# Kernel tuning notes

Hardware: AMD Instinct MI355X
Metric: run time of the kernel (lower is better)

## Reference

```python
import jax, jax.numpy as jnp
import numpy as np

EMBED_DIM = 1024
NUM_HEADS = 16
HEAD_DIM = EMBED_DIM // NUM_HEADS
SEQ = 2048
BATCH = 2


def setup_inputs() -> dict:
    key = jax.random.key(0)
    ks = jax.random.split(key, 8)
    s = 1.0 / np.sqrt(EMBED_DIM)
    return {
        "query": jax.random.normal(ks[0], (SEQ, BATCH, EMBED_DIM), jnp.float32),
        "key": jax.random.normal(ks[1], (SEQ, BATCH, EMBED_DIM), jnp.float32),
        "value": jax.random.normal(ks[2], (SEQ, BATCH, EMBED_DIM), jnp.float32),
        "Wq": jax.random.normal(ks[3], (EMBED_DIM, EMBED_DIM), jnp.float32) * s,
        "Wk": jax.random.normal(ks[4], (EMBED_DIM, EMBED_DIM), jnp.float32) * s,
        "Wv": jax.random.normal(ks[5], (EMBED_DIM, EMBED_DIM), jnp.float32) * s,
        "in_bias": jnp.zeros((3 * EMBED_DIM,), jnp.float32),
        "Wo": jax.random.normal(ks[6], (EMBED_DIM, EMBED_DIM), jnp.float32) * s,
        "bo": jnp.zeros((EMBED_DIM,), jnp.float32),
    }


def reference(query, key, value, Wq, Wk, Wv, in_bias, Wo, bo):
    E, H, D = EMBED_DIM, NUM_HEADS, HEAD_DIM
    # seq-first -> batch-first: [T,B,E] -> [B,T,E]
    q_in = jnp.transpose(query, (1, 0, 2))
    k_in = jnp.transpose(key, (1, 0, 2))
    v_in = jnp.transpose(value, (1, 0, 2))
    B, T, _ = q_in.shape

    # fused in-projection (torch _in_projection: x @ W.T + b)
    q = q_in @ Wq.T + in_bias[:E]
    k = k_in @ Wk.T + in_bias[E:2 * E]
    v = v_in @ Wv.T + in_bias[2 * E:]

    # split heads: [B,T,E] -> [B,H,T,D]
    def split_heads(x):
        return jnp.transpose(x.reshape(B, T, H, D), (0, 2, 1, 3))

    q, k, v = split_heads(q), split_heads(k), split_heads(v)

    # multi-linear (causal linear) attention with outer-product KV state:
    # kv_store[b,h,t] = sum_{s<=t} k_s (outer) v_s        -> [B,H,T,D,D]
    kv_store = jnp.cumsum(jnp.einsum("bhtk,bhtv->bhtkv", k, v), axis=2)
    scale = 1.0 / np.sqrt(D)
    attn = jnp.einsum("bhtk,bhtkv->bhtv", q, kv_store) * scale  # [B,H,T,D]

    # merge heads + out projection
    out = jnp.transpose(attn, (0, 2, 1, 3)).reshape(B, T, E)
    out = out @ Wo.T + bo
    # batch-first -> seq-first
    return jnp.transpose(out, (1, 0, 2))
```

## Files before the change

### kernel.cpp

```cpp
#include <hip/hip_runtime.h>


#define TSEQ 2048
#define BBATCH 2
#define EE 1024
#define TOK 4096
#define NCH 32

typedef _Float16 half8 __attribute__((ext_vector_type(8)));
typedef _Float16 half4 __attribute__((ext_vector_type(4)));
typedef float f32x4 __attribute__((ext_vector_type(4)));

#ifndef __has_builtin
#define __has_builtin(x) 0
#endif
#if __has_builtin(__builtin_amdgcn_global_load_lds)
#define USE_GLL 1
#endif

#ifdef USE_GLL
typedef __attribute__((address_space(1))) const unsigned int guint_t;
typedef __attribute__((address_space(3))) unsigned int luint_t;
#endif

__global__ __launch_bounds__(256) void pack_x_kernel(
    const float* __restrict__ q, const float* __restrict__ k,
    const float* __restrict__ v,
    _Float16* __restrict__ xq, _Float16* __restrict__ xk,
    _Float16* __restrict__ xv) {
  const int blk = blockIdx.x;
  const int m = blk >> 12;
  const int row = blk & 4095;
  const int b = row >> 11, t = row & 2047;
  const float* src = (m == 0 ? q : (m == 1 ? k : v)) +
                     (size_t)t * (BBATCH * EE) + (size_t)b * EE;
  _Float16* dst = (m == 0 ? xq : (m == 1 ? xk : xv)) + (size_t)row * EE;
  const int e = threadIdx.x * 4;
  f32x4 f = *(const f32x4*)&src[e];
  half4 h;
  h[0] = (_Float16)f[0]; h[1] = (_Float16)f[1];
  h[2] = (_Float16)f[2]; h[3] = (_Float16)f[3];
  *(half4*)&dst[e] = h;
}

__global__ __launch_bounds__(256) void pack_w_kernel(
    const float* __restrict__ wq, const float* __restrict__ wk,
    const float* __restrict__ wv, const float* __restrict__ wo,
    _Float16* __restrict__ wb) {
  const int blk = blockIdx.x;
  const int m = blk >> 10, row = blk & 1023;
  const float* src =
      (m == 0 ? wq : (m == 1 ? wk : (m == 2 ? wv : wo))) + (size_t)row * EE;
  _Float16* dst = wb + (size_t)m * EE * EE + (size_t)row * EE;
  const int e = threadIdx.x * 4;
  f32x4 f = *(const f32x4*)&src[e];
  half4 h;
  h[0] = (_Float16)f[0]; h[1] = (_Float16)f[1];
  h[2] = (_Float16)f[2]; h[3] = (_Float16)f[3];
  *(half4*)&dst[e] = h;
}

__device__ __forceinline__ void stage_tile(
    const _Float16* __restrict__ A, const _Float16* __restrict__ Bm,
    long arow0, long brow0, int k0, int tid, int w,
    _Float16* __restrict__ Ab, _Float16* __restrict__ Bb) {
#pragma unroll
  for (int i = 0; i < 4; ++i) {
    const int flat = i * 256 + tid;
    const int r = flat >> 3, s = flat & 7;
    const int c = (s ^ (r & 7)) * 8;
    const _Float16* ga = &A[(size_t)(arow0 + r) * 1024 + k0 + c];
    const _Float16* gb = &Bm[(size_t)(brow0 + r) * 1024 + k0 + c];
#ifdef USE_GLL
    const int ubase = (i * 256 + w * 64) * 8;
    __builtin_amdgcn_global_load_lds((guint_t*)ga, (luint_t*)&Ab[ubase], 16, 0,
                                     0);
    __builtin_amdgcn_global_load_lds((guint_t*)gb, (luint_t*)&Bb[ubase], 16, 0,
                                     0);
#else
    *(half8*)&Ab[flat * 8] = *(const half8*)ga;
    *(half8*)&Bb[flat * 8] = *(const half8*)gb;
#endif
  }
}

__device__ __forceinline__ void gemm_core(
    const _Float16* __restrict__ A, const _Float16* __restrict__ Bm,
    long arow0, long brow0, int tid, f32x4 (&acc)[4][4],
    _Float16 (&Ab)[2][8192], _Float16 (&Bb)[2][8192]) {
  const int lane = tid & 63, w = tid >> 6;
  const int wr = w >> 1, wc = w & 1;
  const int l15 = lane & 15, lg = lane >> 4;
  const int swz = l15 & 7;

#ifdef USE_GLL
  stage_tile(A, Bm, arow0, brow0, 0, tid, w, Ab[0], Bb[0]);
  for (int kt = 0; kt < 16; ++kt) {
    const int cur = kt & 1;
    if (kt < 15) {
      stage_tile(A, Bm, arow0, brow0, (kt + 1) * 64, tid, w, Ab[cur ^ 1],
                 Bb[cur ^ 1]);
      asm volatile("s_waitcnt vmcnt(8)" ::: "memory");
    } else {
      asm volatile("s_waitcnt vmcnt(0)" ::: "memory");
    }
    __builtin_amdgcn_s_barrier();
    asm volatile("" ::: "memory");
#pragma unroll
    for (int ks = 0; ks < 2; ++ks) {
      half8 af[4], bf[4];
#pragma unroll
      for (int mi = 0; mi < 4; ++mi)
        af[mi] = *(const half8*)&Ab[cur][(wr * 64 + mi * 16 + l15) * 64 +
                                         ((ks * 4 + lg) ^ swz) * 8];
#pragma unroll
      for (int ni = 0; ni < 4; ++ni)
        bf[ni] = *(const half8*)&Bb[cur][(wc * 64 + ni * 16 + l15) * 64 +
                                         ((ks * 4 + lg) ^ swz) * 8];
#pragma unroll
      for (int mi = 0; mi < 4; ++mi)
#pragma unroll
        for (int ni = 0; ni < 4; ++ni)
          acc[mi][ni] = __builtin_amdgcn_mfma_f32_16x16x32_f16(
              af[mi], bf[ni], acc[mi][ni], 0, 0, 0);
    }
    asm volatile("" ::: "memory");
    __builtin_amdgcn_s_barrier();
  }
#else
  for (int kt = 0; kt < 16; ++kt) {
    __syncthreads();
    stage_tile(A, Bm, arow0, brow0, kt * 64, tid, w, Ab[0], Bb[0]);
    __syncthreads();
#pragma unroll
    for (int ks = 0; ks < 2; ++ks) {
      half8 af[4], bf[4];
#pragma unroll
      for (int mi = 0; mi < 4; ++mi)
        af[mi] = *(const half8*)&Ab[0][(wr * 64 + mi * 16 + l15) * 64 +
                                       ((ks * 4 + lg) ^ swz) * 8];
#pragma unroll
      for (int ni = 0; ni < 4; ++ni)
        bf[ni] = *(const half8*)&Bb[0][(wc * 64 + ni * 16 + l15) * 64 +
                                       ((ks * 4 + lg) ^ swz) * 8];
#pragma unroll
      for (int mi = 0; mi < 4; ++mi)
#pragma unroll
        for (int ni = 0; ni < 4; ++ni)
          acc[mi][ni] = __builtin_amdgcn_mfma_f32_16x16x32_f16(
              af[mi], bf[ni], acc[mi][ni], 0, 0, 0);
    }
  }
#endif
}

__global__ __launch_bounds__(256) void gemm_inproj(
    const _Float16* __restrict__ X, const _Float16* __restrict__ WB,
    const float* __restrict__ bias, _Float16* __restrict__ Qb,
    _Float16* __restrict__ Kbf, _Float16* __restrict__ KT,
    _Float16* __restrict__ VT) {
  __shared__ __align__(16) _Float16 Ab[2][8192];
  __shared__ __align__(16) _Float16 Bb[2][8192];
  const int tid = threadIdx.x;
  const int which = blockIdx.x >> 3;
  const long arow0 = (long)blockIdx.y * 128;
  const long brow0 = (long)(blockIdx.x & 7) * 128;
  const _Float16* A = X + (size_t)which * (TOK * EE);
  const _Float16* Bm = WB + (size_t)which * (EE * EE);
  const float* bs = bias + which * EE;

  f32x4 acc[4][4] = {};
  gemm_core(A, Bm, arow0, brow0, tid, acc, Ab, Bb);

  const int lane = tid & 63, w = tid >> 6;
  const int wr = w >> 1, wc = w & 1;
  const int l15 = lane & 15, lg = lane >> 4;
#pragma unroll
  for (int mi = 0; mi < 4; ++mi) {
#pragma unroll
    for (int ni = 0; ni < 4; ++ni) {
      const long gm = arow0 + wr * 64 + mi * 16 + lg * 4;
      const long gn = brow0 + wc * 64 + ni * 16 + l15;
      const float bv = bs[gn];
      float vv[4];
#pragma unroll
      for (int r = 0; r < 4; ++r) vv[r] = acc[mi][ni][r] + bv;
      if (which == 0) {
#pragma unroll
        for (int r = 0; r < 4; ++r)
          Qb[(size_t)(gm + r) * EE + gn] = (_Float16)vv[r];
      } else if (which == 1) {
#pragma unroll
        for (int r = 0; r < 4; ++r)
          Kbf[(size_t)(gm + r) * EE + gn] = (_Float16)vv[r];
        half4 pk;
#pragma unroll
        for (int r = 0; r < 4; ++r) pk[r] = (_Float16)vv[r];
        *(half4*)&KT[(size_t)gn * TOK + gm] = pk;
      } else {
        half4 pk;
#pragma unroll
        for (int r = 0; r < 4; ++r) pk[r] = (_Float16)vv[r];
        *(half4*)&VT[(size_t)gn * TOK + gm] = pk;
      }
    }
  }
}

__global__ __launch_bounds__(256) void gemm_out(
    const _Float16* __restrict__ Wo, const _Float16* __restrict__ ATT,
    const float* __restrict__ bo, float* __restrict__ OF) {
  __shared__ __align__(16) _Float16 Ab[2][8192];
  __shared__ __align__(16) _Float16 Bb[2][8192];
  const int tid = threadIdx.x;
  const long arow0 = (long)blockIdx.y * 128;
  const long brow0 = (long)blockIdx.x * 128;

  f32x4 acc[4][4] = {};
  gemm_core(Wo, ATT, arow0, brow0, tid, acc, Ab, Bb);

  const int lane = tid & 63, w = tid >> 6;
  const int wr = w >> 1, wc = w & 1;
  const int l15 = lane & 15, lg = lane >> 4;
#pragma unroll
  for (int mi = 0; mi < 4; ++mi) {
#pragma unroll
    for (int ni = 0; ni < 4; ++ni) {
      const long gm = arow0 + wr * 64 + mi * 16 + lg * 4;
      const long gn = brow0 + wc * 64 + ni * 16 + l15;
      const int t = (int)(gn & 2047), b2 = (int)(gn >> 11);
      f32x4 res;
#pragma unroll
      for (int r = 0; r < 4; ++r) res[r] = acc[mi][ni][r] + bo[gm + r];
      *(f32x4*)&OF[(size_t)t * (BBATCH * EE) + (size_t)b2 * EE + gm] = res;
    }
  }
}

__global__ __launch_bounds__(64) void chunk_g_kernel(
    const _Float16* __restrict__ KT, const _Float16* __restrict__ VT,
    _Float16* __restrict__ GT) {
  const int c = blockIdx.x & 31, bh = blockIdx.x >> 5;
  const int b = bh >> 4, h = bh & 15;
  const int lane = threadIdx.x, l15 = lane & 15, lg = lane >> 4;
  const long tok0 = (long)b * TSEQ + c * 64;

  half8 af[4][2], bf[4][2];
#pragma unroll
  for (int ma = 0; ma < 4; ++ma)
#pragma unroll
    for (int ks = 0; ks < 2; ++ks) {
      const size_t rowoff = (size_t)(h * 64 + ma * 16 + l15) * TOK + tok0 +
                            ks * 32 + lg * 8;
      af[ma][ks] = *(const half8*)&KT[rowoff];
      bf[ma][ks] = *(const half8*)&VT[rowoff];
    }
  f32x4 acc[4][4] = {};
#pragma unroll
  for (int ks = 0; ks < 2; ++ks)
#pragma unroll
    for (int ma = 0; ma < 4; ++ma)
#pragma unroll
      for (int nb = 0; nb < 4; ++nb)
        acc[ma][nb] = __builtin_amdgcn_mfma_f32_16x16x32_f16(
            af[ma][ks], bf[nb][ks], acc[ma][nb], 0, 0, 0);
  _Float16* g = GT + ((size_t)bh * NCH + c) * 4096;
#pragma unroll
  for (int ma = 0; ma < 4; ++ma)
#pragma unroll
    for (int nb = 0; nb < 4; ++nb) {
      half4 pk;
#pragma unroll
      for (int r = 0; r < 4; ++r) pk[r] = (_Float16)acc[ma][nb][r];
      *(half4*)&g[(nb * 16 + l15) * 64 + ma * 16 + lg * 4] = pk;
    }
}

__global__ __launch_bounds__(256) void scan_kernel(
    const _Float16* __restrict__ GT, _Float16* __restrict__ ST) {
  const int gid = blockIdx.x * 256 + threadIdx.x;
  const int bh = gid >> 12, el = gid & 4095;
  const size_t base = (size_t)bh * NCH * 4096 + el;
  float acc = 0.f;
  for (int c = 0; c < NCH; ++c) {
    ST[base + (size_t)c * 4096] = (_Float16)acc;
    acc += (float)GT[base + (size_t)c * 4096];
  }
}

__global__ __launch_bounds__(64) void attn_chunk_kernel(
    const _Float16* __restrict__ Q, const _Float16* __restrict__ Kb,
    const _Float16* __restrict__ VT, const _Float16* __restrict__ ST,
    _Float16* __restrict__ attn) {
  __shared__ __align__(16) _Float16 sc[64 * 72];
  const int c = blockIdx.x & 31, bh = blockIdx.x >> 5;
  const int b = bh >> 4, h = bh & 15;
  const int lane = threadIdx.x, l15 = lane & 15, lg = lane >> 4;
  const long tok0 = (long)b * TSEQ + c * 64;

  half8 qb[4][2];
#pragma unroll
  for (int nb = 0; nb < 4; ++nb)
#pragma unroll
    for (int ks = 0; ks < 2; ++ks)
      qb[nb][ks] = *(const half8*)&Q[(size_t)(tok0 + nb * 16 + l15) * EE +
                                     h * 64 + ks * 32 + lg * 8];

  f32x4 sT[4][4] = {};
#pragma unroll
  for (int ks = 0; ks < 2; ++ks) {
    half8 kf[4];
#pragma unroll
    for (int ma = 0; ma < 4; ++ma)
      kf[ma] = *(const half8*)&Kb[(size_t)(tok0 + ma * 16 + l15) * EE +
                                  h * 64 + ks * 32 + lg * 8];
#pragma unroll
    for (int ma = 0; ma < 4; ++ma)
#pragma unroll
      for (int nb = 0; nb < 4; ++nb)
        sT[ma][nb] = __builtin_amdgcn_mfma_f32_16x16x32_f16(
            kf[ma], qb[nb][ks], sT[ma][nb], 0, 0, 0);
  }
#pragma unroll
  for (int ma = 0; ma < 4; ++ma)
#pragma unroll
    for (int nb = 0; nb < 4; ++nb) {
      const int tp0 = ma * 16 + lg * 4, t = nb * 16 + l15;
      half4 pk;
#pragma unroll
      for (int r = 0; r < 4; ++r)
        pk[r] = (tp0 + r <= t) ? (_Float16)sT[ma][nb][r] : (_Float16)0.f;
      *(half4*)&sc[t * 72 + tp0] = pk;
    }
  __syncthreads();

  f32x4 o[4][4] = {};
  const _Float16* st = ST + ((size_t)bh * NCH + c) * 4096;
#pragma unroll
  for (int ks = 0; ks < 2; ++ks) {
    half8 sf[4];
#pragma unroll
    for (int ma = 0; ma < 4; ++ma)
      sf[ma] = *(const half8*)&st[(ma * 16 + l15) * 64 + ks * 32 + lg * 8];
#pragma unroll
    for (int ma = 0; ma < 4; ++ma)
#pragma unroll
      for (int nb = 0; nb < 4; ++nb)
        o[ma][nb] = __builtin_amdgcn_mfma_f32_16x16x32_f16(
            sf[ma], qb[nb][ks], o[ma][nb], 0, 0, 0);
  }
#pragma unroll
  for (int ks = 0; ks < 2; ++ks) {
    half8 vf[4], sb[4];
#pragma unroll
    for (int ma = 0; ma < 4; ++ma)
      vf[ma] = *(const half8*)&VT[(size_t)(h * 64 + ma * 16 + l15) * TOK +
                                  tok0 + ks * 32 + lg * 8];
#pragma unroll
    for (int nb = 0; nb < 4; ++nb)
      sb[nb] = *(const half8*)&sc[(nb * 16 + l15) * 72 + ks * 32 + lg * 8];
#pragma unroll
    for (int ma = 0; ma < 4; ++ma)
#pragma unroll
      for (int nb = 0; nb < 4; ++nb)
        o[ma][nb] = __builtin_amdgcn_mfma_f32_16x16x32_f16(
            vf[ma], sb[nb], o[ma][nb], 0, 0, 0);
  }
#pragma unroll
  for (int ma = 0; ma < 4; ++ma)
#pragma unroll
    for (int nb = 0; nb < 4; ++nb) {
      const int t = nb * 16 + l15, d20 = ma * 16 + lg * 4;
      half4 pk;
#pragma unroll
      for (int r = 0; r < 4; ++r) pk[r] = (_Float16)(o[ma][nb][r] * 0.125f);
      *(half4*)&attn[(size_t)(tok0 + t) * EE + h * 64 + d20] = pk;
    }
}

extern "C" void kernel_launch(void* const* d_in, const int* in_sizes, int n_in,
                              void* d_out, int out_size, void* d_ws,
                              size_t ws_size, hipStream_t stream) {
  const float* q = (const float*)d_in[0];
  const float* k = (const float*)d_in[1];
  const float* v = (const float*)d_in[2];
  const float* Wq = (const float*)d_in[3];
  const float* Wk = (const float*)d_in[4];
  const float* Wv = (const float*)d_in[5];
  const float* in_bias = (const float*)d_in[6];
  const float* Wo = (const float*)d_in[7];
  const float* bo = (const float*)d_in[8];
  float* out = (float*)d_out;

  char* ws = (char*)d_ws;
  const size_t MB = 1u << 20;
  _Float16* wb = (_Float16*)(ws + 0 * MB);
  _Float16* xq = (_Float16*)(ws + 8 * MB);
  _Float16* xk = (_Float16*)(ws + 16 * MB);
  _Float16* xv = (_Float16*)(ws + 24 * MB);
  _Float16* Qb = (_Float16*)(ws + 32 * MB);
  _Float16* Kbf = (_Float16*)(ws + 40 * MB);
  _Float16* KT = (_Float16*)(ws + 48 * MB);
  _Float16* VT = (_Float16*)(ws + 56 * MB);
  _Float16* attnb = (_Float16*)(ws + 8 * MB);
  _Float16* GT = (_Float16*)(ws + 16 * MB);
  _Float16* STb = (_Float16*)(ws + 24 * MB);

  pack_x_kernel<<<12288, 256, 0, stream>>>(q, k, v, xq, xk, xv);
  pack_w_kernel<<<4096, 256, 0, stream>>>(Wq, Wk, Wv, Wo, wb);

  dim3 gi(24, 32);
  gemm_inproj<<<gi, 256, 0, stream>>>(xq, wb, in_bias, Qb, Kbf, KT, VT);

  chunk_g_kernel<<<1024, 64, 0, stream>>>(KT, VT, GT);
  scan_kernel<<<512, 256, 0, stream>>>(GT, STb);
  attn_chunk_kernel<<<1024, 64, 0, stream>>>(Qb, Kbf, VT, STb, attnb);

  dim3 go(32, 8);
  gemm_out<<<go, 256, 0, stream>>>(wb + 3145728, attnb, bo, out);
}
```

Measured before the change: 206.7 us.

## Enlarge GEMM tiles to 256x256 with 512 threads and XCD-aware block mapping

Both projection GEMMs move from 128x128 tiles on 256 threads to 256x256 tiles on 512 threads, with each wave holding an 8x4 set of MFMA accumulators. Block indices are remapped so neighbouring tiles that share A or B rows land on the same XCD, improving L2 reuse. The aim is fewer global loads per FLOP and better cache locality. In exchange the grids drop to 192 and 64 blocks, which underfills 256 CUs, and register and LDS pressure rise (64KB LDS per block, one block per CU).

```diff
diff --git a/kernel.cpp b/kernel.cpp
--- a/kernel.cpp
+++ b/kernel.cpp
@@ -60,19 +60,19 @@
   *(half4*)&dst[e] = h;
 }
 
-__device__ __forceinline__ void stage_tile(
+__device__ __forceinline__ void stage256(
     const _Float16* __restrict__ A, const _Float16* __restrict__ Bm,
     long arow0, long brow0, int k0, int tid, int w,
     _Float16* __restrict__ Ab, _Float16* __restrict__ Bb) {
 #pragma unroll
   for (int i = 0; i < 4; ++i) {
-    const int flat = i * 256 + tid;
+    const int flat = i * 512 + tid;
     const int r = flat >> 3, s = flat & 7;
     const int c = (s ^ (r & 7)) * 8;
     const _Float16* ga = &A[(size_t)(arow0 + r) * 1024 + k0 + c];
     const _Float16* gb = &Bm[(size_t)(brow0 + r) * 1024 + k0 + c];
 #ifdef USE_GLL
-    const int ubase = (i * 256 + w * 64) * 8;
+    const int ubase = (i * 512 + w * 64) * 8;
     __builtin_amdgcn_global_load_lds((guint_t*)ga, (luint_t*)&Ab[ubase], 16, 0,
                                      0);
     __builtin_amdgcn_global_load_lds((guint_t*)gb, (luint_t*)&Bb[ubase], 16, 0,
@@ -84,22 +84,22 @@
   }
 }
 
-__device__ __forceinline__ void gemm_core(
+__device__ __forceinline__ void gemm_core256(
     const _Float16* __restrict__ A, const _Float16* __restrict__ Bm,
-    long arow0, long brow0, int tid, f32x4 (&acc)[4][4],
-    _Float16 (&Ab)[2][8192], _Float16 (&Bb)[2][8192]) {
+    long arow0, long brow0, int tid, f32x4 (&acc)[8][4],
+    _Float16 (&Ab)[2][16384], _Float16 (&Bb)[2][16384]) {
   const int lane = tid & 63, w = tid >> 6;
-  const int wr = w >> 1, wc = w & 1;
+  const int wr = w >> 2, wc = w & 3;
   const int l15 = lane & 15, lg = lane >> 4;
   const int swz = l15 & 7;
 
 #ifdef USE_GLL
-  stage_tile(A, Bm, arow0, brow0, 0, tid, w, Ab[0], Bb[0]);
+  stage256(A, Bm, arow0, brow0, 0, tid, w, Ab[0], Bb[0]);
   for (int kt = 0; kt < 16; ++kt) {
     const int cur = kt & 1;
     if (kt < 15) {
-      stage_tile(A, Bm, arow0, brow0, (kt + 1) * 64, tid, w, Ab[cur ^ 1],
-                 Bb[cur ^ 1]);
+      stage256(A, Bm, arow0, brow0, (kt + 1) * 64, tid, w, Ab[cur ^ 1],
+               Bb[cur ^ 1]);
       asm volatile("s_waitcnt vmcnt(8)" ::: "memory");
     } else {
       asm volatile("s_waitcnt vmcnt(0)" ::: "memory");
@@ -108,17 +108,17 @@
     asm volatile("" ::: "memory");
 #pragma unroll
     for (int ks = 0; ks < 2; ++ks) {
-      half8 af[4], bf[4];
-#pragma unroll
-      for (int mi = 0; mi < 4; ++mi)
-        af[mi] = *(const half8*)&Ab[cur][(wr * 64 + mi * 16 + l15) * 64 +
+      half8 af[8], bf[4];
+#pragma unroll
+      for (int mi = 0; mi < 8; ++mi)
+        af[mi] = *(const half8*)&Ab[cur][(wr * 128 + mi * 16 + l15) * 64 +
                                          ((ks * 4 + lg) ^ swz) * 8];
 #pragma unroll
       for (int ni = 0; ni < 4; ++ni)
         bf[ni] = *(const half8*)&Bb[cur][(wc * 64 + ni * 16 + l15) * 64 +
                                          ((ks * 4 + lg) ^ swz) * 8];
 #pragma unroll
-      for (int mi = 0; mi < 4; ++mi)
+      for (int mi = 0; mi < 8; ++mi)
 #pragma unroll
         for (int ni = 0; ni < 4; ++ni)
           acc[mi][ni] = __builtin_amdgcn_mfma_f32_16x16x32_f16(
@@ -130,21 +130,21 @@
 #else
   for (int kt = 0; kt < 16; ++kt) {
     __syncthreads();
-    stage_tile(A, Bm, arow0, brow0, kt * 64, tid, w, Ab[0], Bb[0]);
+    stage256(A, Bm, arow0, brow0, kt * 64, tid, w, Ab[0], Bb[0]);
     __syncthreads();
 #pragma unroll
     for (int ks = 0; ks < 2; ++ks) {
-      half8 af[4], bf[4];
-#pragma unroll
-      for (int mi = 0; mi < 4; ++mi)
-        af[mi] = *(const half8*)&Ab[0][(wr * 64 + mi * 16 + l15) * 64 +
+      half8 af[8], bf[4];
+#pragma unroll
+      for (int mi = 0; mi < 8; ++mi)
+        af[mi] = *(const half8*)&Ab[0][(wr * 128 + mi * 16 + l15) * 64 +
                                        ((ks * 4 + lg) ^ swz) * 8];
 #pragma unroll
       for (int ni = 0; ni < 4; ++ni)
         bf[ni] = *(const half8*)&Bb[0][(wc * 64 + ni * 16 + l15) * 64 +
                                        ((ks * 4 + lg) ^ swz) * 8];
 #pragma unroll
-      for (int mi = 0; mi < 4; ++mi)
+      for (int mi = 0; mi < 8; ++mi)
 #pragma unroll
         for (int ni = 0; ni < 4; ++ni)
           acc[mi][ni] = __builtin_amdgcn_mfma_f32_16x16x32_f16(
@@ -154,32 +154,37 @@
 #endif
 }
 
-__global__ __launch_bounds__(256) void gemm_inproj(
+__global__ __launch_bounds__(512, 1) void gemm_inproj(
     const _Float16* __restrict__ X, const _Float16* __restrict__ WB,
     const float* __restrict__ bias, _Float16* __restrict__ Qb,
     _Float16* __restrict__ Kbf, _Float16* __restrict__ KT,
     _Float16* __restrict__ VT) {
-  __shared__ __align__(16) _Float16 Ab[2][8192];
-  __shared__ __align__(16) _Float16 Bb[2][8192];
+  __shared__ __align__(16) _Float16 Ab[2][16384];
+  __shared__ __align__(16) _Float16 Bb[2][16384];
   const int tid = threadIdx.x;
-  const int which = blockIdx.x >> 3;
-  const long arow0 = (long)blockIdx.y * 128;
-  const long brow0 = (long)(blockIdx.x & 7) * 128;
+  const int bid = blockIdx.x;
+  const int xcd = bid & 7, cid = bid >> 3;
+  const int rr = xcd >> 1, rc = xcd & 1;
+  const int mb = rr * 4 + cid / 6;
+  const int col = rc * 6 + cid % 6;
+  const int which = col >> 2, nb = col & 3;
+  const long arow0 = (long)mb * 256;
+  const long brow0 = (long)nb * 256;
   const _Float16* A = X + (size_t)which * (TOK * EE);
   const _Float16* Bm = WB + (size_t)which * (EE * EE);
   const float* bs = bias + which * EE;
 
-  f32x4 acc[4][4] = {};
-  gemm_core(A, Bm, arow0, brow0, tid, acc, Ab, Bb);
+  f32x4 acc[8][4] = {};
+  gemm_core256(A, Bm, arow0, brow0, tid, acc, Ab, Bb);
 
   const int lane = tid & 63, w = tid >> 6;
-  const int wr = w >> 1, wc = w & 1;
+  const int wr = w >> 2, wc = w & 3;
   const int l15 = lane & 15, lg = lane >> 4;
 #pragma unroll
-  for (int mi = 0; mi < 4; ++mi) {
+  for (int mi = 0; mi < 8; ++mi) {
 #pragma unroll
     for (int ni = 0; ni < 4; ++ni) {
-      const long gm = arow0 + wr * 64 + mi * 16 + lg * 4;
+      const long gm = arow0 + wr * 128 + mi * 16 + lg * 4;
       const long gn = brow0 + wc * 64 + ni * 16 + l15;
       const float bv = bs[gn];
       float vv[4];
@@ -207,26 +212,31 @@
   }
 }
 
-__global__ __launch_bounds__(256) void gemm_out(
+__global__ __launch_bounds__(512, 1) void gemm_out(
     const _Float16* __restrict__ Wo, const _Float16* __restrict__ ATT,
     const float* __restrict__ bo, float* __restrict__ OF) {
-  __shared__ __align__(16) _Float16 Ab[2][8192];
-  __shared__ __align__(16) _Float16 Bb[2][8192];
+  __shared__ __align__(16) _Float16 Ab[2][16384];
+  __shared__ __align__(16) _Float16 Bb[2][16384];
   const int tid = threadIdx.x;
-  const long arow0 = (long)blockIdx.y * 128;
-  const long brow0 = (long)blockIdx.x * 128;
-
-  f32x4 acc[4][4] = {};
-  gemm_core(Wo, ATT, arow0, brow0, tid, acc, Ab, Bb);
+  const int bid = blockIdx.x;
+  const int xcd = bid & 7, cid = bid >> 3;
+  const int rr = xcd >> 2, rc = xcd & 3;
+  const int mb = rr * 2 + cid / 4;
+  const int col = rc * 4 + cid % 4;
+  const long arow0 = (long)mb * 256;
+  const long brow0 = (long)col * 256;
+
+  f32x4 acc[8][4] = {};
+  gemm_core256(Wo, ATT, arow0, brow0, tid, acc, Ab, Bb);
 
   const int lane = tid & 63, w = tid >> 6;
-  const int wr = w >> 1, wc = w & 1;
+  const int wr = w >> 2, wc = w & 3;
   const int l15 = lane & 15, lg = lane >> 4;
 #pragma unroll
-  for (int mi = 0; mi < 4; ++mi) {
+  for (int mi = 0; mi < 8; ++mi) {
 #pragma unroll
     for (int ni = 0; ni < 4; ++ni) {
-      const long gm = arow0 + wr * 64 + mi * 16 + lg * 4;
+      const long gm = arow0 + wr * 128 + mi * 16 + lg * 4;
       const long gn = brow0 + wc * 64 + ni * 16 + l15;
       const int t = (int)(gn & 2047), b2 = (int)(gn >> 11);
       f32x4 res;
@@ -409,13 +419,11 @@
   pack_x_kernel<<<12288, 256, 0, stream>>>(q, k, v, xq, xk, xv);
   pack_w_kernel<<<4096, 256, 0, stream>>>(Wq, Wk, Wv, Wo, wb);
 
-  dim3 gi(24, 32);
-  gemm_inproj<<<gi, 256, 0, stream>>>(xq, wb, in_bias, Qb, Kbf, KT, VT);
+  gemm_inproj<<<192, 512, 0, stream>>>(xq, wb, in_bias, Qb, Kbf, KT, VT);
 
   chunk_g_kernel<<<1024, 64, 0, stream>>>(KT, VT, GT);
   scan_kernel<<<512, 256, 0, stream>>>(GT, STb);
   attn_chunk_kernel<<<1024, 64, 0, stream>>>(Qb, Kbf, VT, STb, attnb);
 
-  dim3 go(32, 8);
-  gemm_out<<<go, 256, 0, stream>>>(wb + 3145728, attnb, bo, out);
-}
+  gemm_out<<<64, 512, 0, stream>>>(wb + 3145728, attnb, bo, out);
+}
```

New measurement: 217.7 us. +5.3%, slower.
